# Performance work log

Measured on AMD Instinct MI355X. Metric: run time of the kernel, lower is better.

## Reference

```python
import jax, jax.numpy as jnp
import numpy as np

B, S, H = 2, 1024, 1024
DFF = 2048
E = 8
TOPK = 2


def setup_inputs() -> dict:
    key = jax.random.key(0)
    ks = jax.random.split(key, 12)
    sc = 0.02
    return {
        "x": jax.random.normal(ks[0], (B, S, H), jnp.float32),
        "gate_w": jax.random.normal(ks[1], (H, E), jnp.float32) * sc,
        "gate_b": jnp.zeros((E,), jnp.float32),
        "w1": jax.random.normal(ks[2], (E, H, DFF), jnp.float32) * sc,
        "b1": jnp.zeros((E, DFF), jnp.float32),
        "w2": jax.random.normal(ks[3], (E, H, DFF), jnp.float32) * sc,
        "b2": jnp.zeros((E, DFF), jnp.float32),
        "wg": jax.random.normal(ks[4], (E, DFF, DFF), jnp.float32) * sc,
        "bg": jnp.zeros((E, DFF), jnp.float32),
        "w3": jax.random.normal(ks[5], (E, DFF, H), jnp.float32) * sc,
        "b3": jnp.zeros((E, H), jnp.float32),
    }


def _expert_ffn(x, w1, b1, w2, b2, wg, bg, w3, b3):
    # FeedForward: out = W3( SiGLU( W1(x) * W2(x) ) )
    x1 = jnp.einsum("bsh,hf->bsf", x, w1) + b1
    x2 = jnp.einsum("bsh,hf->bsf", x, w2) + b2
    z = x1 * x2
    # SiGLU(d_ff, d_ff): silu(Linear(z))
    s = jax.nn.silu(jnp.einsum("bsf,fg->bsg", z, wg) + bg)
    return jnp.einsum("bsg,gh->bsh", s, w3) + b3


def reference(x, gate_w, gate_b, w1, b1, w2, b2, wg, bg, w3, b3):
    logits = jnp.einsum("bsh,he->bse", x, gate_w) + gate_b  # [B,S,E]
    topv, topi = jax.lax.top_k(logits, TOPK)                 # [B,S,K]
    probs = jax.nn.softmax(topv, axis=-1)                    # [B,S,K]
    out = jnp.zeros_like(x)
    for e in range(E):
        # per-token combine weight for expert e (0 if not routed)
        we = jnp.sum(probs * (topi == e), axis=-1)           # [B,S]
        y = _expert_ffn(x, w1[e], b1[e], w2[e], b2[e], wg[e], bg[e], w3[e], b3[e])
        out = out + we[..., None] * y
    return out
```

## Files before the change

### kernel.cpp

```cpp
#include <hip/hip_runtime.h>

#define H 1024
#define DFF 2048
#define NE 8
#define NT 2048
#define NPAIR (NT * 2)

typedef __bf16 bf16;
typedef __bf16 bf16x8 __attribute__((ext_vector_type(8)));
typedef __bf16 bf16x4 __attribute__((ext_vector_type(4)));
typedef float f32x4 __attribute__((ext_vector_type(4)));

__device__ __forceinline__ void async_copy16(const void* g, void* l) {
  __builtin_amdgcn_global_load_lds(
      (const __attribute__((address_space(1))) unsigned int*)g,
      (__attribute__((address_space(3))) unsigned int*)l, 16, 0, 0);
}

__global__ __launch_bounds__(64) void gate_kernel(
    const float* __restrict__ x, const float* __restrict__ gw,
    const float* __restrict__ gb, int* __restrict__ cnt,
    int* __restrict__ topi, float* __restrict__ topw) {
  int t = blockIdx.x;
  int lane = threadIdx.x;
  const float* xr = x + (size_t)t * H;
  float acc[NE];
#pragma unroll
  for (int e = 0; e < NE; ++e) acc[e] = 0.f;
  for (int i = lane; i < H; i += 64) {
    float xv = xr[i];
    const float* g = gw + (size_t)i * NE;
#pragma unroll
    for (int e = 0; e < NE; ++e) acc[e] += xv * g[e];
  }
#pragma unroll
  for (int e = 0; e < NE; ++e) {
    for (int off = 32; off > 0; off >>= 1)
      acc[e] += __shfl_down(acc[e], off, 64);
  }
  if (lane == 0) {
    float v[NE];
#pragma unroll
    for (int e = 0; e < NE; ++e) v[e] = acc[e] + gb[e];
    int i1 = 0;
#pragma unroll
    for (int e = 1; e < NE; ++e) if (v[e] > v[i1]) i1 = e;
    int i2 = (i1 == 0) ? 1 : 0;
#pragma unroll
    for (int e = 0; e < NE; ++e) if (e != i1 && v[e] > v[i2]) i2 = e;
    float d = expf(v[i2] - v[i1]);
    float p1 = 1.f / (1.f + d);
    float p2 = d * p1;
    topi[2 * t] = i1; topi[2 * t + 1] = i2;
    topw[2 * t] = p1; topw[2 * t + 1] = p2;
    atomicAdd(&cnt[i1], 1);
    atomicAdd(&cnt[i2], 1);
  }
}

__global__ void prefix_kernel(const int* __restrict__ cnt, int* __restrict__ off) {
  if (threadIdx.x == 0 && blockIdx.x == 0) {
    int s = 0;
    for (int e = 0; e < NE; ++e) { off[e] = s; s += cnt[e]; }
    off[NE] = s;
  }
}

__global__ __launch_bounds__(256) void scatter_kernel(
    const int* __restrict__ topi, int* __restrict__ cnt2,
    const int* __restrict__ off, int* __restrict__ pair_tok,
    int* __restrict__ pair_pos) {
  int t = blockIdx.x * 256 + threadIdx.x;
  if (t >= NT) return;
#pragma unroll
  for (int k = 0; k < 2; ++k) {
    int e = topi[2 * t + k];
    int idx = atomicAdd(&cnt2[e], 1);
    int pos = off[e] + idx;
    pair_tok[pos] = t;
    pair_pos[2 * t + k] = pos;
  }
}

__global__ __launch_bounds__(256) void conv_x_kernel(const float* __restrict__ in,
                                                     bf16* __restrict__ out) {
  int i = (blockIdx.x * 256 + threadIdx.x) * 4;
  float4 v = *(const float4*)(in + i);
  bf16x4 o = {(bf16)v.x, (bf16)v.y, (bf16)v.z, (bf16)v.w};
  *(bf16x4*)(out + i) = o;
}

#define TP 72
__global__ __launch_bounds__(256) void tconv_kernel(const float* __restrict__ in,
                                                    bf16* __restrict__ out,
                                                    int K, int N) {
  int e = blockIdx.z;
  int k0 = blockIdx.y * 64, n0 = blockIdx.x * 64;
  __shared__ bf16 T[64 * TP];
  const float* src = in + ((size_t)e * K + k0) * N + n0;
  bf16* dst = out + ((size_t)e * N + n0) * K + k0;
  int t = threadIdx.x;
  int ln = (t & 15) * 4, lk = t >> 4;
#pragma unroll
  for (int it = 0; it < 4; ++it) {
    int kk = it * 16 + lk;
    float4 v = *(const float4*)(src + (size_t)kk * N + ln);
    T[(ln + 0) * TP + kk] = (bf16)v.x;
    T[(ln + 1) * TP + kk] = (bf16)v.y;
    T[(ln + 2) * TP + kk] = (bf16)v.z;
    T[(ln + 3) * TP + kk] = (bf16)v.w;
  }
  __syncthreads();
  int sk = (t & 7) * 8, sn = t >> 3;
#pragma unroll
  for (int it = 0; it < 2; ++it) {
    int nn = it * 32 + sn;
    *(bf16x8*)(dst + (size_t)nn * K + sk) = *(const bf16x8*)&T[nn * TP + sk];
  }
}

__global__ __launch_bounds__(256) void ffn1_kernel(
    const bf16* __restrict__ xb, const bf16* __restrict__ w1t,
    const float* __restrict__ b1, const bf16* __restrict__ w2t,
    const float* __restrict__ b2, const int* __restrict__ off,
    const int* __restrict__ pair_tok, bf16* __restrict__ Z) {
  int e = blockIdx.y;
  int base = off[e];
  int count = off[e + 1] - base;
  int m0 = blockIdx.z * 128;
  if (m0 >= count) return;
  int n0 = blockIdx.x * 64;

  __shared__ bf16 As[128 * 32];
  __shared__ bf16 B1s[64 * 32];
  __shared__ bf16 B2s[64 * 32];

  int tid = threadIdx.x;
  int wave = tid >> 6, lane = tid & 63;
  int quad = lane >> 4, l16 = lane & 15;
  int wm = wave & 1, wn = wave >> 1;

  int sr = lane >> 2, sc = lane & 3;
  int chunk = (sc ^ (sr & 3)) * 16;

  int ar0 = m0 + wave * 32 + sr;      if (ar0 >= count) ar0 = count - 1;
  int ar1 = m0 + wave * 32 + 16 + sr; if (ar1 >= count) ar1 = count - 1;
  int tok0 = pair_tok[base + ar0];
  int tok1 = pair_tok[base + ar1];
  const char* ap0 = (const char*)(xb + (size_t)tok0 * H) + chunk;
  const char* ap1 = (const char*)(xb + (size_t)tok1 * H) + chunk;

  const char* w1e = (const char*)(w1t + (size_t)e * DFF * H);
  const char* w2e = (const char*)(w2t + (size_t)e * DFF * H);
  const char* b1p = w1e + (size_t)(n0 + wave * 16 + sr) * H * 2 + chunk;
  const char* b2p = w2e + (size_t)(n0 + wave * 16 + sr) * H * 2 + chunk;

  char* asd  = (char*)As  + wave * 2048;
  char* b1sd = (char*)B1s + wave * 1024;
  char* b2sd = (char*)B2s + wave * 1024;

  int fsw = (quad ^ (l16 & 3)) * 16 + l16 * 64;
  const char* ar = (const char*)As + wm * 4096 + fsw;
  const char* b1r = (const char*)B1s + wn * 2048 + fsw;
  const char* b2r = (const char*)B2s + wn * 2048 + fsw;

  f32x4 acc1[4][2] = {};
  f32x4 acc2[4][2] = {};

  for (int k0 = 0; k0 < H * 2; k0 += 64) {
    async_copy16(ap0 + k0, asd);
    async_copy16(ap1 + k0, asd + 1024);
    async_copy16(b1p + k0, b1sd);
    async_copy16(b2p + k0, b2sd);
    __syncthreads();
    bf16x8 af[4], bf1[2], bf2[2];
#pragma unroll
    for (int i = 0; i < 4; ++i) af[i] = *(const bf16x8*)(ar + i * 1024);
#pragma unroll
    for (int i = 0; i < 2; ++i) bf1[i] = *(const bf16x8*)(b1r + i * 1024);
#pragma unroll
    for (int i = 0; i < 2; ++i) bf2[i] = *(const bf16x8*)(b2r + i * 1024);
#pragma unroll
    for (int fm = 0; fm < 4; ++fm)
#pragma unroll
      for (int fn = 0; fn < 2; ++fn) {
        acc1[fm][fn] = __builtin_amdgcn_mfma_f32_16x16x32_bf16(af[fm], bf1[fn], acc1[fm][fn], 0, 0, 0);
        acc2[fm][fn] = __builtin_amdgcn_mfma_f32_16x16x32_bf16(af[fm], bf2[fn], acc2[fm][fn], 0, 0, 0);
      }
    __syncthreads();
  }

  int mb = m0 + wm * 64;
#pragma unroll
  for (int fm = 0; fm < 4; ++fm) {
#pragma unroll
    for (int fn = 0; fn < 2; ++fn) {
      int n = n0 + wn * 32 + fn * 16 + l16;
      float bb1 = b1[e * DFF + n];
      float bb2 = b2[e * DFF + n];
#pragma unroll
      for (int r = 0; r < 4; ++r) {
        int m = mb + fm * 16 + quad * 4 + r;
        if (m < count) {
          float zv = (acc1[fm][fn][r] + bb1) * (acc2[fm][fn][r] + bb2);
          Z[(size_t)(base + m) * DFF + n] = (bf16)zv;
        }
      }
    }
  }
}

__global__ __launch_bounds__(256) void ffn2_kernel(
    const bf16* __restrict__ Z, const bf16* __restrict__ wgt,
    const float* __restrict__ bg, const int* __restrict__ off,
    bf16* __restrict__ S) {
  int e = blockIdx.y;
  int base = off[e];
  int count = off[e + 1] - base;
  int m0 = blockIdx.z * 128;
  if (m0 >= count) return;
  int n0 = blockIdx.x * 128;

  __shared__ bf16 As[128 * 32];
  __shared__ bf16 Bs[128 * 32];

  int tid = threadIdx.x;
  int wave = tid >> 6, lane = tid & 63;
  int quad = lane >> 4, l16 = lane & 15;
  int wm = wave & 1, wn = wave >> 1;

  int sr = lane >> 2, sc = lane & 3;
  int chunk = (sc ^ (sr & 3)) * 16;

  int ar0 = m0 + wave * 32 + sr;      if (ar0 >= count) ar0 = count - 1;
  int ar1 = m0 + wave * 32 + 16 + sr; if (ar1 >= count) ar1 = count - 1;
  const char* ap0 = (const char*)(Z + (size_t)(base + ar0) * DFF) + chunk;
  const char* ap1 = (const char*)(Z + (size_t)(base + ar1) * DFF) + chunk;

  const char* we = (const char*)(wgt + (size_t)e * DFF * DFF);
  const char* bp0 = we + (size_t)(n0 + wave * 32 + sr) * DFF * 2 + chunk;
  const char* bp1 = we + (size_t)(n0 + wave * 32 + 16 + sr) * DFF * 2 + chunk;

  char* asd = (char*)As + wave * 2048;
  char* bsd = (char*)Bs + wave * 2048;

  int fsw = (quad ^ (l16 & 3)) * 16 + l16 * 64;
  const char* ar = (const char*)As + wm * 4096 + fsw;
  const char* br = (const char*)Bs + wn * 4096 + fsw;

  f32x4 acc[4][4] = {};

  for (int k0 = 0; k0 < DFF * 2; k0 += 64) {
    async_copy16(ap0 + k0, asd);
    async_copy16(ap1 + k0, asd + 1024);
    async_copy16(bp0 + k0, bsd);
    async_copy16(bp1 + k0, bsd + 1024);
    __syncthreads();
    bf16x8 af[4], bfr[4];
#pragma unroll
    for (int i = 0; i < 4; ++i) af[i] = *(const bf16x8*)(ar + i * 1024);
#pragma unroll
    for (int i = 0; i < 4; ++i) bfr[i] = *(const bf16x8*)(br + i * 1024);
#pragma unroll
    for (int fm = 0; fm < 4; ++fm)
#pragma unroll
      for (int fn = 0; fn < 4; ++fn)
        acc[fm][fn] = __builtin_amdgcn_mfma_f32_16x16x32_bf16(af[fm], bfr[fn], acc[fm][fn], 0, 0, 0);
    __syncthreads();
  }

  int mb = m0 + wm * 64;
#pragma unroll
  for (int fm = 0; fm < 4; ++fm) {
#pragma unroll
    for (int fn = 0; fn < 4; ++fn) {
      int n = n0 + wn * 64 + fn * 16 + l16;
      float bb = bg[e * DFF + n];
#pragma unroll
      for (int r = 0; r < 4; ++r) {
        int m = mb + fm * 16 + quad * 4 + r;
        if (m < count) {
          float v = acc[fm][fn][r] + bb;
          S[(size_t)(base + m) * DFF + n] = (bf16)(v / (1.f + __expf(-v)));
        }
      }
    }
  }
}

__global__ __launch_bounds__(256) void ffn3_kernel(
    const bf16* __restrict__ S, const bf16* __restrict__ w3t,
    const float* __restrict__ b3, const int* __restrict__ off,
    bf16* __restrict__ Y) {
  int e = blockIdx.y;
  int base = off[e];
  int count = off[e + 1] - base;
  int m0 = blockIdx.z * 128;
  if (m0 >= count) return;
  int n0 = blockIdx.x * 64;

  __shared__ bf16 As[128 * 32];
  __shared__ bf16 Bs[64 * 32];

  int tid = threadIdx.x;
  int wave = tid >> 6, lane = tid & 63;
  int quad = lane >> 4, l16 = lane & 15;
  int wm = wave & 1, wn = wave >> 1;

  int sr = lane >> 2, sc = lane & 3;
  int chunk = (sc ^ (sr & 3)) * 16;

  int ar0 = m0 + wave * 32 + sr;      if (ar0 >= count) ar0 = count - 1;
  int ar1 = m0 + wave * 32 + 16 + sr; if (ar1 >= count) ar1 = count - 1;
  const char* ap0 = (const char*)(S + (size_t)(base + ar0) * DFF) + chunk;
  const char* ap1 = (const char*)(S + (size_t)(base + ar1) * DFF) + chunk;

  const char* we = (const char*)(w3t + (size_t)e * H * DFF);
  const char* bp0 = we + (size_t)(n0 + wave * 16 + sr) * DFF * 2 + chunk;

  char* asd = (char*)As + wave * 2048;
  char* bsd = (char*)Bs + wave * 1024;

  int fsw = (quad ^ (l16 & 3)) * 16 + l16 * 64;
  const char* ar = (const char*)As + wm * 4096 + fsw;
  const char* br = (const char*)Bs + wn * 2048 + fsw;

  f32x4 acc[4][2] = {};

  for (int k0 = 0; k0 < DFF * 2; k0 += 64) {
    async_copy16(ap0 + k0, asd);
    async_copy16(ap1 + k0, asd + 1024);
    async_copy16(bp0 + k0, bsd);
    __syncthreads();
    bf16x8 af[4], bfr[2];
#pragma unroll
    for (int i = 0; i < 4; ++i) af[i] = *(const bf16x8*)(ar + i * 1024);
#pragma unroll
    for (int i = 0; i < 2; ++i) bfr[i] = *(const bf16x8*)(br + i * 1024);
#pragma unroll
    for (int fm = 0; fm < 4; ++fm)
#pragma unroll
      for (int fn = 0; fn < 2; ++fn)
        acc[fm][fn] = __builtin_amdgcn_mfma_f32_16x16x32_bf16(af[fm], bfr[fn], acc[fm][fn], 0, 0, 0);
    __syncthreads();
  }

  int mb = m0 + wm * 64;
#pragma unroll
  for (int fm = 0; fm < 4; ++fm) {
#pragma unroll
    for (int fn = 0; fn < 2; ++fn) {
      int n = n0 + wn * 32 + fn * 16 + l16;
      float bb = b3[e * H + n];
#pragma unroll
      for (int r = 0; r < 4; ++r) {
        int m = mb + fm * 16 + quad * 4 + r;
        if (m < count) {
          Y[(size_t)(base + m) * H + n] = (bf16)(acc[fm][fn][r] + bb);
        }
      }
    }
  }
}

__global__ __launch_bounds__(256) void combine_kernel(
    const bf16* __restrict__ Y, const int* __restrict__ pair_pos,
    const float* __restrict__ topw, float* __restrict__ out) {
  int idx = blockIdx.x * 256 + threadIdx.x;
  int t = idx >> 8;
  int h4 = idx & 255;
  int p0 = pair_pos[2 * t], p1 = pair_pos[2 * t + 1];
  float w0 = topw[2 * t], w1 = topw[2 * t + 1];
  bf16x4 a = *(const bf16x4*)(Y + (size_t)p0 * H + h4 * 4);
  bf16x4 b = *(const bf16x4*)(Y + (size_t)p1 * H + h4 * 4);
  float4 o;
  o.x = w0 * (float)a[0] + w1 * (float)b[0];
  o.y = w0 * (float)a[1] + w1 * (float)b[1];
  o.z = w0 * (float)a[2] + w1 * (float)b[2];
  o.w = w0 * (float)a[3] + w1 * (float)b[3];
  ((float4*)out)[idx] = o;
}

extern "C" void kernel_launch(void* const* d_in, const int* in_sizes, int n_in,
                              void* d_out, int out_size, void* d_ws, size_t ws_size,
                              hipStream_t stream) {
  const float* x  = (const float*)d_in[0];
  const float* gw = (const float*)d_in[1];
  const float* gb = (const float*)d_in[2];
  const float* w1 = (const float*)d_in[3];
  const float* b1 = (const float*)d_in[4];
  const float* w2 = (const float*)d_in[5];
  const float* b2 = (const float*)d_in[6];
  const float* wg = (const float*)d_in[7];
  const float* bg = (const float*)d_in[8];
  const float* w3 = (const float*)d_in[9];
  const float* b3 = (const float*)d_in[10];
  float* out = (float*)d_out;

  char* ws = (char*)d_ws;
  int* cnt      = (int*)(ws + 0);
  int* cnt2     = (int*)(ws + 64);
  int* off      = (int*)(ws + 128);
  int* topi     = (int*)(ws + 4096);
  float* topw   = (float*)(ws + 4096 + 16384);
  int* pair_tok = (int*)(ws + 4096 + 16384 * 2);
  int* pair_pos = (int*)(ws + 4096 + 16384 * 3);

  const size_t MB = 1024 * 1024;
  char* big = ws + MB;
  bf16* xb  = (bf16*)(big);
  bf16* w1t = (bf16*)(big + 4   * MB);
  bf16* w2t = (bf16*)(big + 36  * MB);
  bf16* wgt = (bf16*)(big + 68  * MB);
  bf16* w3t = (bf16*)(big + 132 * MB);
  bf16* Z   = (bf16*)(big + 164 * MB);
  bf16* S   = (bf16*)(big + 180 * MB);
  bf16* Y   = (bf16*)(big + 196 * MB);

  hipMemsetAsync(d_ws, 0, 256, stream);
  gate_kernel<<<NT, 64, 0, stream>>>(x, gw, gb, cnt, topi, topw);
  prefix_kernel<<<1, 64, 0, stream>>>(cnt, off);
  scatter_kernel<<<NT / 256, 256, 0, stream>>>(topi, cnt2, off, pair_tok, pair_pos);

  conv_x_kernel<<<NT * H / 1024, 256, 0, stream>>>(x, xb);
  tconv_kernel<<<dim3(DFF / 64, H / 64,  NE), 256, 0, stream>>>(w1, w1t, H,  DFF);
  tconv_kernel<<<dim3(DFF / 64, H / 64,  NE), 256, 0, stream>>>(w2, w2t, H,  DFF);
  tconv_kernel<<<dim3(DFF / 64, DFF / 64, NE), 256, 0, stream>>>(wg, wgt, DFF, DFF);
  tconv_kernel<<<dim3(H / 64,  DFF / 64, NE), 256, 0, stream>>>(w3, w3t, DFF, H);

  ffn1_kernel<<<dim3(DFF / 64, NE, NPAIR / 128), 256, 0, stream>>>(xb, w1t, b1, w2t, b2, off, pair_tok, Z);
  ffn2_kernel<<<dim3(DFF / 128, NE, NPAIR / 128), 256, 0, stream>>>(Z, wgt, bg, off, S);
  ffn3_kernel<<<dim3(H / 64, NE, NPAIR / 128), 256, 0, stream>>>(S, w3t, b3, off, Y);
  combine_kernel<<<(NT * H / 4) / 256, 256, 0, stream>>>(Y, pair_pos, topw, out);
}
```

Measured before the change: 609.4 us.

## Double K-tile depth in expert GEMMs, fuse x conversion and weight transposes

The three expert GEMM kernels now stage a 64-wide K slice per iteration instead of 32, using a new 8-way XOR swizzle, so each pair of barriers covers twice as many MFMAs. The x-to-bf16 conversion moves into the gate kernel, and the four weight transpose launches merge into one launch that dispatches on block index. The aim is to cut barrier and loop overhead and launch count, at the cost of doubled shared memory per block, which may lower occupancy. The transpose kernel now stages fp32 in LDS and converts on the way out.

```diff
diff --git a/kernel.cpp b/kernel.cpp
--- a/kernel.cpp
+++ b/kernel.cpp
@@ -20,10 +20,19 @@
 __global__ __launch_bounds__(64) void gate_kernel(
     const float* __restrict__ x, const float* __restrict__ gw,
     const float* __restrict__ gb, int* __restrict__ cnt,
-    int* __restrict__ topi, float* __restrict__ topw) {
+    int* __restrict__ topi, float* __restrict__ topw,
+    bf16* __restrict__ xb) {
   int t = blockIdx.x;
   int lane = threadIdx.x;
   const float* xr = x + (size_t)t * H;
+  bf16* xbr = xb + (size_t)t * H;
+#pragma unroll
+  for (int it = 0; it < 4; ++it) {
+    int i = it * 256 + lane * 4;
+    float4 v = *(const float4*)(xr + i);
+    bf16x4 o = {(bf16)v.x, (bf16)v.y, (bf16)v.z, (bf16)v.w};
+    *(bf16x4*)(xbr + i) = o;
+  }
   float acc[NE];
 #pragma unroll
   for (int e = 0; e < NE; ++e) acc[e] = 0.f;
@@ -82,42 +91,51 @@
   }
 }
 
-__global__ __launch_bounds__(256) void conv_x_kernel(const float* __restrict__ in,
-                                                     bf16* __restrict__ out) {
-  int i = (blockIdx.x * 256 + threadIdx.x) * 4;
-  float4 v = *(const float4*)(in + i);
-  bf16x4 o = {(bf16)v.x, (bf16)v.y, (bf16)v.z, (bf16)v.w};
-  *(bf16x4*)(out + i) = o;
-}
-
-#define TP 72
-__global__ __launch_bounds__(256) void tconv_kernel(const float* __restrict__ in,
-                                                    bf16* __restrict__ out,
-                                                    int K, int N) {
-  int e = blockIdx.z;
-  int k0 = blockIdx.y * 64, n0 = blockIdx.x * 64;
-  __shared__ bf16 T[64 * TP];
-  const float* src = in + ((size_t)e * K + k0) * N + n0;
-  bf16* dst = out + ((size_t)e * N + n0) * K + k0;
+__global__ __launch_bounds__(256) void tconv_kernel(
+    const float* __restrict__ w1, const float* __restrict__ w2,
+    const float* __restrict__ wg, const float* __restrict__ w3,
+    bf16* __restrict__ w1t, bf16* __restrict__ w2t,
+    bf16* __restrict__ wgt, bf16* __restrict__ w3t) {
+  int bid = blockIdx.x;
+  const float* src; bf16* dst; int K, N, e, kt, nt;
+  if (bid < 8192) {
+    if (bid < 4096) { src = w1; dst = w1t; } else { src = w2; dst = w2t; bid -= 4096; }
+    K = H; N = DFF;
+    e = bid >> 9; int l = bid & 511; kt = l >> 5; nt = l & 31;
+  } else if (bid < 16384) {
+    src = wg; dst = wgt; K = DFF; N = DFF;
+    int l = bid - 8192; e = l >> 10; l &= 1023; kt = l >> 5; nt = l & 31;
+  } else {
+    src = w3; dst = w3t; K = DFF; N = H;
+    int l = bid - 16384; e = l >> 9; l &= 511; kt = l >> 4; nt = l & 15;
+  }
+  src += ((size_t)e * K + kt * 64) * N + nt * 64;
+  dst += ((size_t)e * N + nt * 64) * K + kt * 64;
+
+  __shared__ float T[64 * 65];
   int t = threadIdx.x;
-  int ln = (t & 15) * 4, lk = t >> 4;
+  int n4 = (t & 15) * 4, kk = t >> 4;
 #pragma unroll
   for (int it = 0; it < 4; ++it) {
-    int kk = it * 16 + lk;
-    float4 v = *(const float4*)(src + (size_t)kk * N + ln);
-    T[(ln + 0) * TP + kk] = (bf16)v.x;
-    T[(ln + 1) * TP + kk] = (bf16)v.y;
-    T[(ln + 2) * TP + kk] = (bf16)v.z;
-    T[(ln + 3) * TP + kk] = (bf16)v.w;
+    int k = it * 16 + kk;
+    float4 v = *(const float4*)(src + (size_t)k * N + n4);
+    T[(n4 + 0) * 65 + k] = v.x;
+    T[(n4 + 1) * 65 + k] = v.y;
+    T[(n4 + 2) * 65 + k] = v.z;
+    T[(n4 + 3) * 65 + k] = v.w;
   }
   __syncthreads();
-  int sk = (t & 7) * 8, sn = t >> 3;
+  int k8 = (t & 7) * 8, n = t >> 3;
 #pragma unroll
   for (int it = 0; it < 2; ++it) {
-    int nn = it * 32 + sn;
-    *(bf16x8*)(dst + (size_t)nn * K + sk) = *(const bf16x8*)&T[nn * TP + sk];
-  }
-}
+    int nn = it * 32 + n;
+    const float* row = &T[nn * 65 + k8];
+    bf16x8 o = {(bf16)row[0], (bf16)row[1], (bf16)row[2], (bf16)row[3],
+                (bf16)row[4], (bf16)row[5], (bf16)row[6], (bf16)row[7]};
+    *(bf16x8*)(dst + (size_t)nn * K + k8) = o;
+  }
+}
+
 
 __global__ __launch_bounds__(256) void ffn1_kernel(
     const bf16* __restrict__ xb, const bf16* __restrict__ w1t,
@@ -131,62 +149,74 @@
   if (m0 >= count) return;
   int n0 = blockIdx.x * 64;
 
-  __shared__ bf16 As[128 * 32];
-  __shared__ bf16 B1s[64 * 32];
-  __shared__ bf16 B2s[64 * 32];
+  __shared__ __align__(16) bf16 As[128 * 64];
+  __shared__ __align__(16) bf16 B1s[64 * 64];
+  __shared__ __align__(16) bf16 B2s[64 * 64];
 
   int tid = threadIdx.x;
   int wave = tid >> 6, lane = tid & 63;
   int quad = lane >> 4, l16 = lane & 15;
   int wm = wave & 1, wn = wave >> 1;
-
-  int sr = lane >> 2, sc = lane & 3;
-  int chunk = (sc ^ (sr & 3)) * 16;
-
-  int ar0 = m0 + wave * 32 + sr;      if (ar0 >= count) ar0 = count - 1;
-  int ar1 = m0 + wave * 32 + 16 + sr; if (ar1 >= count) ar1 = count - 1;
-  int tok0 = pair_tok[base + ar0];
-  int tok1 = pair_tok[base + ar1];
-  const char* ap0 = (const char*)(xb + (size_t)tok0 * H) + chunk;
-  const char* ap1 = (const char*)(xb + (size_t)tok1 * H) + chunk;
-
+  int lr = lane >> 3, lc = lane & 7;
+  int cg = (lc ^ lr) * 16;
+
+  const char* apj[4];
+#pragma unroll
+  for (int j = 0; j < 4; ++j) {
+    int r = m0 + wave * 32 + j * 8 + lr;
+    if (r >= count) r = count - 1;
+    apj[j] = (const char*)(xb + (size_t)pair_tok[base + r] * H) + cg;
+  }
   const char* w1e = (const char*)(w1t + (size_t)e * DFF * H);
   const char* w2e = (const char*)(w2t + (size_t)e * DFF * H);
-  const char* b1p = w1e + (size_t)(n0 + wave * 16 + sr) * H * 2 + chunk;
-  const char* b2p = w2e + (size_t)(n0 + wave * 16 + sr) * H * 2 + chunk;
-
-  char* asd  = (char*)As  + wave * 2048;
-  char* b1sd = (char*)B1s + wave * 1024;
-  char* b2sd = (char*)B2s + wave * 1024;
-
-  int fsw = (quad ^ (l16 & 3)) * 16 + l16 * 64;
-  const char* ar = (const char*)As + wm * 4096 + fsw;
-  const char* b1r = (const char*)B1s + wn * 2048 + fsw;
-  const char* b2r = (const char*)B2s + wn * 2048 + fsw;
+  const char* b1pj[2];
+  const char* b2pj[2];
+#pragma unroll
+  for (int j = 0; j < 2; ++j) {
+    int r = n0 + wave * 16 + j * 8 + lr;
+    b1pj[j] = w1e + (size_t)r * (H * 2) + cg;
+    b2pj[j] = w2e + (size_t)r * (H * 2) + cg;
+  }
+
+  char* asd  = (char*)As  + wave * 4096;
+  char* b1sd = (char*)B1s + wave * 2048;
+  char* b2sd = (char*)B2s + wave * 2048;
+
+  int slot0 = ((0 + quad) ^ (l16 & 7)) * 16;
+  int slot1 = ((4 + quad) ^ (l16 & 7)) * 16;
+  const char* arp  = (const char*)As  + (wm * 64 + l16) * 128;
+  const char* b1rp = (const char*)B1s + (wn * 32 + l16) * 128;
+  const char* b2rp = (const char*)B2s + (wn * 32 + l16) * 128;
 
   f32x4 acc1[4][2] = {};
   f32x4 acc2[4][2] = {};
 
-  for (int k0 = 0; k0 < H * 2; k0 += 64) {
-    async_copy16(ap0 + k0, asd);
-    async_copy16(ap1 + k0, asd + 1024);
-    async_copy16(b1p + k0, b1sd);
-    async_copy16(b2p + k0, b2sd);
-    __syncthreads();
-    bf16x8 af[4], bf1[2], bf2[2];
-#pragma unroll
-    for (int i = 0; i < 4; ++i) af[i] = *(const bf16x8*)(ar + i * 1024);
-#pragma unroll
-    for (int i = 0; i < 2; ++i) bf1[i] = *(const bf16x8*)(b1r + i * 1024);
-#pragma unroll
-    for (int i = 0; i < 2; ++i) bf2[i] = *(const bf16x8*)(b2r + i * 1024);
-#pragma unroll
-    for (int fm = 0; fm < 4; ++fm)
-#pragma unroll
-      for (int fn = 0; fn < 2; ++fn) {
-        acc1[fm][fn] = __builtin_amdgcn_mfma_f32_16x16x32_bf16(af[fm], bf1[fn], acc1[fm][fn], 0, 0, 0);
-        acc2[fm][fn] = __builtin_amdgcn_mfma_f32_16x16x32_bf16(af[fm], bf2[fn], acc2[fm][fn], 0, 0, 0);
-      }
+  for (int k0 = 0; k0 < H * 2; k0 += 128) {
+#pragma unroll
+    for (int j = 0; j < 4; ++j) async_copy16(apj[j] + k0, asd + j * 1024);
+#pragma unroll
+    for (int j = 0; j < 2; ++j) async_copy16(b1pj[j] + k0, b1sd + j * 1024);
+#pragma unroll
+    for (int j = 0; j < 2; ++j) async_copy16(b2pj[j] + k0, b2sd + j * 1024);
+    __syncthreads();
+#pragma unroll
+    for (int ks = 0; ks < 2; ++ks) {
+      int slot = ks ? slot1 : slot0;
+      bf16x8 af[4], bf1[2], bf2[2];
+#pragma unroll
+      for (int i = 0; i < 4; ++i) af[i] = *(const bf16x8*)(arp + i * 2048 + slot);
+#pragma unroll
+      for (int i = 0; i < 2; ++i) bf1[i] = *(const bf16x8*)(b1rp + i * 2048 + slot);
+#pragma unroll
+      for (int i = 0; i < 2; ++i) bf2[i] = *(const bf16x8*)(b2rp + i * 2048 + slot);
+#pragma unroll
+      for (int fm = 0; fm < 4; ++fm)
+#pragma unroll
+        for (int fn = 0; fn < 2; ++fn) {
+          acc1[fm][fn] = __builtin_amdgcn_mfma_f32_16x16x32_bf16(af[fm], bf1[fn], acc1[fm][fn], 0, 0, 0);
+          acc2[fm][fn] = __builtin_amdgcn_mfma_f32_16x16x32_bf16(af[fm], bf2[fn], acc2[fm][fn], 0, 0, 0);
+        }
+    }
     __syncthreads();
   }
 
@@ -221,51 +251,58 @@
   if (m0 >= count) return;
   int n0 = blockIdx.x * 128;
 
-  __shared__ bf16 As[128 * 32];
-  __shared__ bf16 Bs[128 * 32];
+  __shared__ __align__(16) bf16 As[128 * 64];
+  __shared__ __align__(16) bf16 Bs[128 * 64];
 
   int tid = threadIdx.x;
   int wave = tid >> 6, lane = tid & 63;
   int quad = lane >> 4, l16 = lane & 15;
   int wm = wave & 1, wn = wave >> 1;
-
-  int sr = lane >> 2, sc = lane & 3;
-  int chunk = (sc ^ (sr & 3)) * 16;
-
-  int ar0 = m0 + wave * 32 + sr;      if (ar0 >= count) ar0 = count - 1;
-  int ar1 = m0 + wave * 32 + 16 + sr; if (ar1 >= count) ar1 = count - 1;
-  const char* ap0 = (const char*)(Z + (size_t)(base + ar0) * DFF) + chunk;
-  const char* ap1 = (const char*)(Z + (size_t)(base + ar1) * DFF) + chunk;
-
+  int lr = lane >> 3, lc = lane & 7;
+  int cg = (lc ^ lr) * 16;
+
+  const char* apj[4];
+  const char* bpj[4];
   const char* we = (const char*)(wgt + (size_t)e * DFF * DFF);
-  const char* bp0 = we + (size_t)(n0 + wave * 32 + sr) * DFF * 2 + chunk;
-  const char* bp1 = we + (size_t)(n0 + wave * 32 + 16 + sr) * DFF * 2 + chunk;
-
-  char* asd = (char*)As + wave * 2048;
-  char* bsd = (char*)Bs + wave * 2048;
-
-  int fsw = (quad ^ (l16 & 3)) * 16 + l16 * 64;
-  const char* ar = (const char*)As + wm * 4096 + fsw;
-  const char* br = (const char*)Bs + wn * 4096 + fsw;
+#pragma unroll
+  for (int j = 0; j < 4; ++j) {
+    int r = m0 + wave * 32 + j * 8 + lr;
+    if (r >= count) r = count - 1;
+    apj[j] = (const char*)(Z + (size_t)(base + r) * DFF) + cg;
+    int rb = n0 + wave * 32 + j * 8 + lr;
+    bpj[j] = we + (size_t)rb * (DFF * 2) + cg;
+  }
+
+  char* asd = (char*)As + wave * 4096;
+  char* bsd = (char*)Bs + wave * 4096;
+
+  int slot0 = ((0 + quad) ^ (l16 & 7)) * 16;
+  int slot1 = ((4 + quad) ^ (l16 & 7)) * 16;
+  const char* arp = (const char*)As + (wm * 64 + l16) * 128;
+  const char* brp = (const char*)Bs + (wn * 64 + l16) * 128;
 
   f32x4 acc[4][4] = {};
 
-  for (int k0 = 0; k0 < DFF * 2; k0 += 64) {
-    async_copy16(ap0 + k0, asd);
-    async_copy16(ap1 + k0, asd + 1024);
-    async_copy16(bp0 + k0, bsd);
-    async_copy16(bp1 + k0, bsd + 1024);
-    __syncthreads();
-    bf16x8 af[4], bfr[4];
-#pragma unroll
-    for (int i = 0; i < 4; ++i) af[i] = *(const bf16x8*)(ar + i * 1024);
-#pragma unroll
-    for (int i = 0; i < 4; ++i) bfr[i] = *(const bf16x8*)(br + i * 1024);
-#pragma unroll
-    for (int fm = 0; fm < 4; ++fm)
-#pragma unroll
-      for (int fn = 0; fn < 4; ++fn)
-        acc[fm][fn] = __builtin_amdgcn_mfma_f32_16x16x32_bf16(af[fm], bfr[fn], acc[fm][fn], 0, 0, 0);
+  for (int k0 = 0; k0 < DFF * 2; k0 += 128) {
+#pragma unroll
+    for (int j = 0; j < 4; ++j) async_copy16(apj[j] + k0, asd + j * 1024);
+#pragma unroll
+    for (int j = 0; j < 4; ++j) async_copy16(bpj[j] + k0, bsd + j * 1024);
+    __syncthreads();
+#pragma unroll
+    for (int ks = 0; ks < 2; ++ks) {
+      int slot = ks ? slot1 : slot0;
+      bf16x8 af[4], bfr[4];
+#pragma unroll
+      for (int i = 0; i < 4; ++i) af[i] = *(const bf16x8*)(arp + i * 2048 + slot);
+#pragma unroll
+      for (int i = 0; i < 4; ++i) bfr[i] = *(const bf16x8*)(brp + i * 2048 + slot);
+#pragma unroll
+      for (int fm = 0; fm < 4; ++fm)
+#pragma unroll
+        for (int fn = 0; fn < 4; ++fn)
+          acc[fm][fn] = __builtin_amdgcn_mfma_f32_16x16x32_bf16(af[fm], bfr[fn], acc[fm][fn], 0, 0, 0);
+    }
     __syncthreads();
   }
 
@@ -299,49 +336,61 @@
   if (m0 >= count) return;
   int n0 = blockIdx.x * 64;
 
-  __shared__ bf16 As[128 * 32];
-  __shared__ bf16 Bs[64 * 32];
+  __shared__ __align__(16) bf16 As[128 * 64];
+  __shared__ __align__(16) bf16 Bs[64 * 64];
 
   int tid = threadIdx.x;
   int wave = tid >> 6, lane = tid & 63;
   int quad = lane >> 4, l16 = lane & 15;
   int wm = wave & 1, wn = wave >> 1;
-
-  int sr = lane >> 2, sc = lane & 3;
-  int chunk = (sc ^ (sr & 3)) * 16;
-
-  int ar0 = m0 + wave * 32 + sr;      if (ar0 >= count) ar0 = count - 1;
-  int ar1 = m0 + wave * 32 + 16 + sr; if (ar1 >= count) ar1 = count - 1;
-  const char* ap0 = (const char*)(S + (size_t)(base + ar0) * DFF) + chunk;
-  const char* ap1 = (const char*)(S + (size_t)(base + ar1) * DFF) + chunk;
-
+  int lr = lane >> 3, lc = lane & 7;
+  int cg = (lc ^ lr) * 16;
+
+  const char* apj[4];
+#pragma unroll
+  for (int j = 0; j < 4; ++j) {
+    int r = m0 + wave * 32 + j * 8 + lr;
+    if (r >= count) r = count - 1;
+    apj[j] = (const char*)(S + (size_t)(base + r) * DFF) + cg;
+  }
   const char* we = (const char*)(w3t + (size_t)e * H * DFF);
-  const char* bp0 = we + (size_t)(n0 + wave * 16 + sr) * DFF * 2 + chunk;
-
-  char* asd = (char*)As + wave * 2048;
-  char* bsd = (char*)Bs + wave * 1024;
-
-  int fsw = (quad ^ (l16 & 3)) * 16 + l16 * 64;
-  const char* ar = (const char*)As + wm * 4096 + fsw;
-  const char* br = (const char*)Bs + wn * 2048 + fsw;
+  const char* bpj[2];
+#pragma unroll
+  for (int j = 0; j < 2; ++j) {
+    int r = n0 + wave * 16 + j * 8 + lr;
+    bpj[j] = we + (size_t)r * (DFF * 2) + cg;
+  }
+
+  char* asd = (char*)As + wave * 4096;
+  char* bsd = (char*)Bs + wave * 2048;
+
+  int slot0 = ((0 + quad) ^ (l16 & 7)) * 16;
+  int slot1 = ((4 + quad) ^ (l16 & 7)) * 16;
+  const char* arp = (const char*)As + (wm * 64 + l16) * 128;
+  const char* brp = (const char*)Bs + (wn * 32 + l16) * 128;
 
   f32x4 acc[4][2] = {};
 
-  for (int k0 = 0; k0 < DFF * 2; k0 += 64) {
-    async_copy16(ap0 + k0, asd);
-    async_copy16(ap1 + k0, asd + 1024);
-    async_copy16(bp0 + k0, bsd);
-    __syncthreads();
-    bf16x8 af[4], bfr[2];
-#pragma unroll
-    for (int i = 0; i < 4; ++i) af[i] = *(const bf16x8*)(ar + i * 1024);
-#pragma unroll
-    for (int i = 0; i < 2; ++i) bfr[i] = *(const bf16x8*)(br + i * 1024);
-#pragma unroll
-    for (int fm = 0; fm < 4; ++fm)
-#pragma unroll
-      for (int fn = 0; fn < 2; ++fn)
-        acc[fm][fn] = __builtin_amdgcn_mfma_f32_16x16x32_bf16(af[fm], bfr[fn], acc[fm][fn], 0, 0, 0);
+  for (int k0 = 0; k0 < DFF * 2; k0 += 128) {
+#pragma unroll
+    for (int j = 0; j < 4; ++j) async_copy16(apj[j] + k0, asd + j * 1024);
+#pragma unroll
+    for (int j = 0; j < 2; ++j) async_copy16(bpj[j] + k0, bsd + j * 1024);
+    __syncthreads();
+#pragma unroll
+    for (int ks = 0; ks < 2; ++ks) {
+      int slot = ks ? slot1 : slot0;
+      bf16x8 af[4], bfr[2];
+#pragma unroll
+      for (int i = 0; i < 4; ++i) af[i] = *(const bf16x8*)(arp + i * 2048 + slot);
+#pragma unroll
+      for (int i = 0; i < 2; ++i) bfr[i] = *(const bf16x8*)(brp + i * 2048 + slot);
+#pragma unroll
+      for (int fm = 0; fm < 4; ++fm)
+#pragma unroll
+        for (int fn = 0; fn < 2; ++fn)
+          acc[fm][fn] = __builtin_amdgcn_mfma_f32_16x16x32_bf16(af[fm], bfr[fn], acc[fm][fn], 0, 0, 0);
+    }
     __syncthreads();
   }
 
@@ -418,15 +467,11 @@
   bf16* Y   = (bf16*)(big + 196 * MB);
 
   hipMemsetAsync(d_ws, 0, 256, stream);
-  gate_kernel<<<NT, 64, 0, stream>>>(x, gw, gb, cnt, topi, topw);
+  gate_kernel<<<NT, 64, 0, stream>>>(x, gw, gb, cnt, topi, topw, xb);
   prefix_kernel<<<1, 64, 0, stream>>>(cnt, off);
   scatter_kernel<<<NT / 256, 256, 0, stream>>>(topi, cnt2, off, pair_tok, pair_pos);
 
-  conv_x_kernel<<<NT * H / 1024, 256, 0, stream>>>(x, xb);
-  tconv_kernel<<<dim3(DFF / 64, H / 64,  NE), 256, 0, stream>>>(w1, w1t, H,  DFF);
-  tconv_kernel<<<dim3(DFF / 64, H / 64,  NE), 256, 0, stream>>>(w2, w2t, H,  DFF);
-  tconv_kernel<<<dim3(DFF / 64, DFF / 64, NE), 256, 0, stream>>>(wg, wgt, DFF, DFF);
-  tconv_kernel<<<dim3(H / 64,  DFF / 64, NE), 256, 0, stream>>>(w3, w3t, DFF, H);
+  tconv_kernel<<<20480, 256, 0, stream>>>(w1, w2, wg, w3, w1t, w2t, wgt, w3t);
 
   ffn1_kernel<<<dim3(DFF / 64, NE, NPAIR / 128), 256, 0, stream>>>(xb, w1t, b1, w2t, b2, off, pair_tok, Z);
   ffn2_kernel<<<dim3(DFF / 128, NE, NPAIR / 128), 256, 0, stream>>>(Z, wgt, bg, off, S);
```

After: 626.3 us. +2.8%, slower.
